# Kernel optimization log

Hardware: AMD Instinct MI355X
Metric: run time of the kernel (lower is better)

The kernel has to match this reference:

```python
import jax, jax.numpy as jnp
import numpy as np

B, T, D, H = 2, 4096, 768, 12
HD = D // H  # head_dim = 64


def setup_inputs() -> dict:
    key = jax.random.key(0)
    ks = jax.random.split(key, 6)
    s = 0.02
    return {
        "x": jax.random.normal(ks[0], (B, T, D), dtype=jnp.float32),
        "Wq": jax.random.normal(ks[1], (D, D), dtype=jnp.float32) * s,
        "Wk": jax.random.normal(ks[2], (D, D), dtype=jnp.float32) * s,
        "Wv": jax.random.normal(ks[3], (D, D), dtype=jnp.float32) * s,
        "Wo": jax.random.normal(ks[4], (D, D), dtype=jnp.float32) * s,
        "bo": jnp.zeros((D,), dtype=jnp.float32),
    }


def reference(x, Wq, Wk, Wv, Wo, bo):
    b, t, d = x.shape
    # QKV projections (no bias), reshape to [B, H, T, HD]
    def heads(w):
        return (x @ w.T).reshape(b, t, H, HD).transpose(0, 2, 1, 3)
    q, k, v = heads(Wq), heads(Wk), heads(Wv)
    scores = jnp.einsum("bhqd,bhkd->bhqk", q, k)  # [B,H,T,T]
    causal = jnp.tril(jnp.ones((t, t), dtype=bool))
    scores = jnp.where(causal, scores, -jnp.inf)
    attn = jax.nn.softmax(scores / jnp.sqrt(jnp.float32(HD)), axis=-1)
    ctx = jnp.einsum("bhqk,bhkd->bhqd", attn, v)  # [B,H,T,HD]
    ctx = ctx.transpose(0, 2, 1, 3).reshape(b, t, d)
    return ctx @ Wo.T + bo
```

## Files before the change

### kernel.cpp

```cpp
#include <hip/hip_runtime.h>
#include <hip/hip_bf16.h>
#include <cstdint>
#include <cstddef>

#define B_  2
#define T_  4096
#define D_  768
#define H_  12
#define HD_ 64
#define M_  (B_*T_)

#define SCL 0.18033688f

typedef __bf16 bf16x8 __attribute__((ext_vector_type(8)));
typedef float  f32x4  __attribute__((ext_vector_type(4)));
using bf16 = __hip_bfloat16;

__device__ inline float fexp2(float x) {
  float r; asm("v_exp_f32 %0, %1" : "=v"(r) : "v"(x)); return r;
}
__device__ inline uint32_t pkbf(float a, float b) {
  union { bf16 h[2]; uint32_t u; } x;
  x.h[0] = __float2bfloat16(a); x.h[1] = __float2bfloat16(b);
  return x.u;
}
#define GLD16(g, l) __builtin_amdgcn_global_load_lds( \
    (const __attribute__((address_space(1))) uint32_t*)(const void*)(g), \
    (__attribute__((address_space(3))) uint32_t*)(void*)(l), 16, 0, 0)

__global__ void cvt_x_kernel(const float* __restrict__ src, bf16* __restrict__ dst, int n4) {
  int i = blockIdx.x * blockDim.x + threadIdx.x;
  if (i < n4) {
    float4 v = ((const float4*)src)[i];
    union { bf16 o[4]; uint2 u; } pk;
    pk.o[0] = __float2bfloat16(v.x); pk.o[1] = __float2bfloat16(v.y);
    pk.o[2] = __float2bfloat16(v.z); pk.o[3] = __float2bfloat16(v.w);
    *(uint2*)(dst + 4 * (size_t)i) = pk.u;
  }
}

__global__ void cvt_w_kernel(const float* __restrict__ s0, const float* __restrict__ s1,
                             const float* __restrict__ s2, const float* __restrict__ s3,
                             bf16* __restrict__ d0, bf16* __restrict__ d1,
                             bf16* __restrict__ d2, bf16* __restrict__ d3, int n4) {
  const float* s; bf16* d;
  switch (blockIdx.y) {
    case 0: s = s0; d = d0; break;
    case 1: s = s1; d = d1; break;
    case 2: s = s2; d = d2; break;
    default: s = s3; d = d3; break;
  }
  int i = blockIdx.x * blockDim.x + threadIdx.x;
  if (i < n4) {
    float4 v = ((const float4*)s)[i];
    union { bf16 o[4]; uint2 u; } pk;
    pk.o[0] = __float2bfloat16(v.x); pk.o[1] = __float2bfloat16(v.y);
    pk.o[2] = __float2bfloat16(v.z); pk.o[3] = __float2bfloat16(v.w);
    *(uint2*)(d + 4 * (size_t)i) = pk.u;
  }
}

__global__ __launch_bounds__(256) void gemm_qkv(const bf16* __restrict__ A,
                                                const bf16* __restrict__ W0,
                                                const bf16* __restrict__ W1,
                                                const bf16* __restrict__ W2,
                                                bf16* __restrict__ O0,
                                                bf16* __restrict__ O1,
                                                bf16* __restrict__ O2t) {
  __shared__ bf16 As[128 * 40];
  __shared__ bf16 Bs[128 * 40];
  const int z = blockIdx.z;
  const bf16* Bw = (z == 0) ? W0 : ((z == 1) ? W1 : W2);
  const int t  = threadIdx.x;
  const int m0 = blockIdx.y * 128;
  const int n0 = blockIdx.x * 128;
  const int wid = t >> 6, lane = t & 63;
  const int wm = (wid >> 1) * 64, wn = (wid & 1) * 64;
  const int mi = lane & 15, qd = lane >> 4;

  f32x4 acc[4][4] = {};

  for (int k0 = 0; k0 < 768; k0 += 32) {
    __syncthreads();
    #pragma unroll
    for (int c = 0; c < 2; ++c) {
      int q   = t + 256 * c;
      int row = q >> 2, c16 = q & 3;
      uint4 va = *(const uint4*)(A  + (size_t)(m0 + row) * 768 + k0 + c16 * 8);
      *(uint4*)(As + row * 40 + c16 * 8) = va;
      uint4 vb = *(const uint4*)(Bw + (size_t)(n0 + row) * 768 + k0 + c16 * 8);
      *(uint4*)(Bs + row * 40 + c16 * 8) = vb;
    }
    __syncthreads();
    bf16x8 af[4], bfr[4];
    #pragma unroll
    for (int mt = 0; mt < 4; ++mt)
      af[mt] = *(const bf16x8*)(As + (wm + mt * 16 + mi) * 40 + qd * 8);
    #pragma unroll
    for (int nt = 0; nt < 4; ++nt)
      bfr[nt] = *(const bf16x8*)(Bs + (wn + nt * 16 + mi) * 40 + qd * 8);
    #pragma unroll
    for (int mt = 0; mt < 4; ++mt)
      #pragma unroll
      for (int nt = 0; nt < 4; ++nt)
        acc[mt][nt] = __builtin_amdgcn_mfma_f32_16x16x32_bf16(af[mt], bfr[nt], acc[mt][nt], 0, 0, 0);
  }

  const float scl = (z == 1) ? SCL : 1.0f;
  bf16* Ob = (z == 0) ? O0 : O1;
  #pragma unroll
  for (int mt = 0; mt < 4; ++mt) {
    #pragma unroll
    for (int nt = 0; nt < 4; ++nt) {
      int gr0 = m0 + wm + mt * 16 + qd * 4;
      int gc  = n0 + wn + nt * 16 + mi;
      if (z == 2) {
        union { bf16 o[4]; uint2 u; } pk;
        #pragma unroll
        for (int r = 0; r < 4; ++r) pk.o[r] = __float2bfloat16(acc[mt][nt][r]);
        int bb = gr0 >> 12, tt = gr0 & 4095;
        *(uint2*)(O2t + (size_t)bb * 768 * 4096 + (size_t)gc * 4096 + tt) = pk.u;
      } else {
        #pragma unroll
        for (int r = 0; r < 4; ++r)
          Ob[(size_t)(gr0 + r) * 768 + gc] = __float2bfloat16(acc[mt][nt][r] * scl);
      }
    }
  }
}

__global__ __launch_bounds__(256) void gemm_out(const bf16* __restrict__ A,
                                                const bf16* __restrict__ Bw,
                                                float* __restrict__ Cf,
                                                const float* __restrict__ bias) {
  __shared__ bf16 As[128 * 40];
  __shared__ bf16 Bs[128 * 40];
  const int t  = threadIdx.x;
  const int m0 = blockIdx.y * 128;
  const int n0 = blockIdx.x * 128;
  const int wid = t >> 6, lane = t & 63;
  const int wm = (wid >> 1) * 64, wn = (wid & 1) * 64;
  const int mi = lane & 15, qd = lane >> 4;

  f32x4 acc[4][4] = {};

  for (int k0 = 0; k0 < 768; k0 += 32) {
    __syncthreads();
    #pragma unroll
    for (int c = 0; c < 2; ++c) {
      int q   = t + 256 * c;
      int row = q >> 2, c16 = q & 3;
      uint4 va = *(const uint4*)(A  + (size_t)(m0 + row) * 768 + k0 + c16 * 8);
      *(uint4*)(As + row * 40 + c16 * 8) = va;
      uint4 vb = *(const uint4*)(Bw + (size_t)(n0 + row) * 768 + k0 + c16 * 8);
      *(uint4*)(Bs + row * 40 + c16 * 8) = vb;
    }
    __syncthreads();
    bf16x8 af[4], bfr[4];
    #pragma unroll
    for (int mt = 0; mt < 4; ++mt)
      af[mt] = *(const bf16x8*)(As + (wm + mt * 16 + mi) * 40 + qd * 8);
    #pragma unroll
    for (int nt = 0; nt < 4; ++nt)
      bfr[nt] = *(const bf16x8*)(Bs + (wn + nt * 16 + mi) * 40 + qd * 8);
    #pragma unroll
    for (int mt = 0; mt < 4; ++mt)
      #pragma unroll
      for (int nt = 0; nt < 4; ++nt)
        acc[mt][nt] = __builtin_amdgcn_mfma_f32_16x16x32_bf16(af[mt], bfr[nt], acc[mt][nt], 0, 0, 0);
  }

  #pragma unroll
  for (int mt = 0; mt < 4; ++mt)
    #pragma unroll
    for (int nt = 0; nt < 4; ++nt) {
      int gr0 = m0 + wm + mt * 16 + qd * 4;
      int gc  = n0 + wn + nt * 16 + mi;
      #pragma unroll
      for (int r = 0; r < 4; ++r)
        Cf[(size_t)(gr0 + r) * 768 + gc] = acc[mt][nt][r] + bias[gc];
    }
}

__global__ __launch_bounds__(256) void flash_attn(const bf16* __restrict__ Q,
                                                  const bf16* __restrict__ K,
                                                  const bf16* __restrict__ Vt,
                                                  bf16* __restrict__ ctx) {
  __shared__ bf16 Ks[2][4096];
  __shared__ bf16 Vs[2][4096];
  __shared__ bf16 Pt[4][32 * 72];
  const int t = threadIdx.x;
  const int w = t >> 6, lane = t & 63;
  const int mi = lane & 15, qd = lane >> 4;
  const int bh   = blockIdx.x % 24;
  const int qrev = blockIdx.x / 24;
  const int q0 = T_ - 128 - qrev * 128;
  const int b = bh / H_, h = bh % H_;
  const size_t bTD = (size_t)b * T_ * D_;
  const char* Kp = (const char*)(K  + bTD + (size_t)h * HD_);
  const char* Vp = (const char*)(Vt + (size_t)b * D_ * T_ + (size_t)h * HD_ * T_);
  const int qwmin = q0 + w * 32;

  int vkoff[2], vvoff[2];
  #pragma unroll
  for (int i = 0; i < 2; ++i) {
    int s  = i * 64 + lane;
    int rl = s >> 3, cs = s & 7;
    int c  = cs ^ (rl & 7);
    vkoff[i] = (w * 16 + rl) * 1536 + c * 16;
    vvoff[i] = (w * 16 + rl) * 8192 + c * 16;
  }

  int fidx[4][2];
  #pragma unroll
  for (int jt = 0; jt < 4; ++jt)
    #pragma unroll
    for (int kt = 0; kt < 2; ++kt)
      fidx[jt][kt] = (jt * 16 + mi) * 64 + (((kt * 4 + qd) ^ (mi & 7)) * 8);

  bf16x8 qf[2][2];
  const bf16* Qp = Q + bTD + (size_t)h * HD_;
  #pragma unroll
  for (int qt = 0; qt < 2; ++qt)
    #pragma unroll
    for (int kt = 0; kt < 2; ++kt)
      qf[qt][kt] = *(const bf16x8*)(Qp + (size_t)(qwmin + qt * 16 + mi) * D_ + kt * 32 + qd * 8);

  f32x4 oacc[4][2] = {};
  float lst[2] = {0.f, 0.f};

  const int ntiles = q0 / 64 + 2;

  #pragma unroll
  for (int i = 0; i < 2; ++i) {
    GLD16(Kp + vkoff[i], &Ks[0][w * 1024 + i * 512]);
    GLD16(Vp + vvoff[i], &Vs[0][w * 1024 + i * 512]);
  }

  for (int tt = 0; tt < ntiles; ++tt) {
    __syncthreads();
    const int par = tt & 1;
    if (tt + 1 < ntiles) {
      const size_t j1 = (size_t)(tt + 1) * 64;
      const int np = par ^ 1;
      #pragma unroll
      for (int i = 0; i < 2; ++i) {
        GLD16(Kp + vkoff[i] + j1 * 1536, &Ks[np][w * 1024 + i * 512]);
        GLD16(Vp + vvoff[i] + j1 * 2,    &Vs[np][w * 1024 + i * 512]);
      }
    }
    const int j0 = tt * 64;
    if (j0 > qwmin + 31) continue;

    f32x4 sacc[4][2] = {};
    #pragma unroll
    for (int jt = 0; jt < 4; ++jt)
      #pragma unroll
      for (int kt = 0; kt < 2; ++kt) {
        bf16x8 kf = *(const bf16x8*)&Ks[par][fidx[jt][kt]];
        #pragma unroll
        for (int qt = 0; qt < 2; ++qt)
          sacc[jt][qt] = __builtin_amdgcn_mfma_f32_16x16x32_bf16(kf, qf[qt][kt], sacc[jt][qt], 0, 0, 0);
      }

    if (j0 + 63 > qwmin) {
      #pragma unroll
      for (int jt = 0; jt < 4; ++jt)
        #pragma unroll
        for (int qt = 0; qt < 2; ++qt) {
          int qg = qwmin + qt * 16 + mi;
          #pragma unroll
          for (int r = 0; r < 4; ++r) {
            int jg = j0 + jt * 16 + qd * 4 + r;
            if (jg > qg) sacc[jt][qt][r] = -1e30f;
          }
        }
    }

    #pragma unroll
    for (int jt = 0; jt < 4; ++jt)
      #pragma unroll
      for (int qt = 0; qt < 2; ++qt) {
        float p0 = fexp2(sacc[jt][qt][0]);
        float p1 = fexp2(sacc[jt][qt][1]);
        float p2 = fexp2(sacc[jt][qt][2]);
        float p3 = fexp2(sacc[jt][qt][3]);
        lst[qt] += (p0 + p1) + (p2 + p3);
        union { uint32_t u[2]; uint64_t d; } pw;
        pw.u[0] = pkbf(p0, p1);
        pw.u[1] = pkbf(p2, p3);
        *(uint64_t*)&Pt[w][(qt * 16 + mi) * 72 + jt * 16 + qd * 4] = pw.d;
      }

    bf16x8 vf[4][2];
    #pragma unroll
    for (int dt = 0; dt < 4; ++dt)
      #pragma unroll
      for (int kt = 0; kt < 2; ++kt)
        vf[dt][kt] = *(const bf16x8*)&Vs[par][fidx[dt][kt]];

    asm volatile("s_waitcnt lgkmcnt(0)" ::: "memory");

    #pragma unroll
    for (int ktp = 0; ktp < 2; ++ktp)
      #pragma unroll
      for (int qt = 0; qt < 2; ++qt) {
        bf16x8 pf = *(const bf16x8*)&Pt[w][(qt * 16 + mi) * 72 + ktp * 32 + qd * 8];
        #pragma unroll
        for (int dt = 0; dt < 4; ++dt)
          oacc[dt][qt] = __builtin_amdgcn_mfma_f32_16x16x32_bf16(vf[dt][ktp], pf, oacc[dt][qt], 0, 0, 0);
      }
  }

  #pragma unroll
  for (int qt = 0; qt < 2; ++qt) {
    float l = lst[qt];
    l += __shfl_xor(l, 16);
    l += __shfl_xor(l, 32);
    float inv = __builtin_amdgcn_rcpf(l);
    int qg = qwmin + qt * 16 + mi;
    bf16* cp = ctx + bTD + (size_t)qg * D_ + h * HD_ + qd * 4;
    #pragma unroll
    for (int dt = 0; dt < 4; ++dt) {
      union { bf16 o[4]; uint2 u; } pko;
      #pragma unroll
      for (int r = 0; r < 4; ++r) pko.o[r] = __float2bfloat16(oacc[dt][qt][r] * inv);
      *(uint2*)(cp + dt * 16) = pko.u;
    }
  }
}

extern "C" void kernel_launch(void* const* d_in, const int* in_sizes, int n_in,
                              void* d_out, int out_size, void* d_ws, size_t ws_size,
                              hipStream_t stream) {
  const float* x  = (const float*)d_in[0];
  const float* Wq = (const float*)d_in[1];
  const float* Wk = (const float*)d_in[2];
  const float* Wv = (const float*)d_in[3];
  const float* Wo = (const float*)d_in[4];
  const float* bo = (const float*)d_in[5];
  float* out = (float*)d_out;

  char* ws = (char*)d_ws;
  const size_t SZ  = (size_t)M_ * D_ * 2;
  const size_t WSZ = (size_t)D_ * D_ * 2;
  bf16* xb   = (bf16*)(ws);
  bf16* Qb   = (bf16*)(ws + 1 * SZ);
  bf16* Kb   = (bf16*)(ws + 2 * SZ);
  bf16* Vtg  = (bf16*)(ws + 3 * SZ);
  bf16* ctxb = (bf16*)(ws + 4 * SZ);
  bf16* Wqb  = (bf16*)(ws + 5 * SZ);
  bf16* Wkb  = (bf16*)(ws + 5 * SZ + 1 * WSZ);
  bf16* Wvb  = (bf16*)(ws + 5 * SZ + 2 * WSZ);
  bf16* Wob  = (bf16*)(ws + 5 * SZ + 3 * WSZ);

  const int nx4 = M_ * D_ / 4;
  cvt_x_kernel<<<(nx4 + 255) / 256, 256, 0, stream>>>(x, xb, nx4);
  const int nw4 = D_ * D_ / 4;
  dim3 gcw((nw4 + 255) / 256, 4);
  cvt_w_kernel<<<gcw, 256, 0, stream>>>(Wq, Wk, Wv, Wo, Wqb, Wkb, Wvb, Wob, nw4);

  dim3 gq(D_ / 128, M_ / 128, 3);
  gemm_qkv<<<gq, 256, 0, stream>>>(xb, Wqb, Wkb, Wvb, Qb, Kb, Vtg);

  flash_attn<<<(T_ / 128) * B_ * H_, 256, 0, stream>>>(Qb, Kb, Vtg, ctxb);

  dim3 gg(D_ / 128, M_ / 128);
  gemm_out<<<gg, 256, 0, stream>>>(ctxb, Wob, out, bo);
}
```

Measured before the change: 280.9 us.

## Double-buffer GEMM tiles via async global-to-LDS loads, merge conversion kernels

```diff
diff --git a/kernel.cpp b/kernel.cpp
--- a/kernel.cpp
+++ b/kernel.cpp
@@ -19,36 +19,27 @@
 __device__ inline float fexp2(float x) {
   float r; asm("v_exp_f32 %0, %1" : "=v"(r) : "v"(x)); return r;
 }
-__device__ inline uint32_t pkbf(float a, float b) {
-  union { bf16 h[2]; uint32_t u; } x;
-  x.h[0] = __float2bfloat16(a); x.h[1] = __float2bfloat16(b);
-  return x.u;
+__device__ inline uint32_t fu(float x) { union { float f; uint32_t u; } c; c.f = x; return c.u; }
+__device__ inline uint32_t pktr(float a, float b) {
+  return __builtin_amdgcn_perm(fu(b), fu(a), 0x07060302);
 }
 #define GLD16(g, l) __builtin_amdgcn_global_load_lds( \
     (const __attribute__((address_space(1))) uint32_t*)(const void*)(g), \
     (__attribute__((address_space(3))) uint32_t*)(void*)(l), 16, 0, 0)
 
-__global__ void cvt_x_kernel(const float* __restrict__ src, bf16* __restrict__ dst, int n4) {
-  int i = blockIdx.x * blockDim.x + threadIdx.x;
-  if (i < n4) {
-    float4 v = ((const float4*)src)[i];
-    union { bf16 o[4]; uint2 u; } pk;
-    pk.o[0] = __float2bfloat16(v.x); pk.o[1] = __float2bfloat16(v.y);
-    pk.o[2] = __float2bfloat16(v.z); pk.o[3] = __float2bfloat16(v.w);
-    *(uint2*)(dst + 4 * (size_t)i) = pk.u;
-  }
-}
-
-__global__ void cvt_w_kernel(const float* __restrict__ s0, const float* __restrict__ s1,
-                             const float* __restrict__ s2, const float* __restrict__ s3,
-                             bf16* __restrict__ d0, bf16* __restrict__ d1,
-                             bf16* __restrict__ d2, bf16* __restrict__ d3, int n4) {
-  const float* s; bf16* d;
+__global__ void cvt_all(const float* __restrict__ x,
+                        const float* __restrict__ w0, const float* __restrict__ w1,
+                        const float* __restrict__ w2, const float* __restrict__ w3,
+                        bf16* __restrict__ xd,
+                        bf16* __restrict__ d0, bf16* __restrict__ d1,
+                        bf16* __restrict__ d2, bf16* __restrict__ d3) {
+  const float* s; bf16* d; int n4;
   switch (blockIdx.y) {
-    case 0: s = s0; d = d0; break;
-    case 1: s = s1; d = d1; break;
-    case 2: s = s2; d = d2; break;
-    default: s = s3; d = d3; break;
+    case 0: s = x;  d = xd; n4 = M_ * D_ / 4; break;
+    case 1: s = w0; d = d0; n4 = D_ * D_ / 4; break;
+    case 2: s = w1; d = d1; n4 = D_ * D_ / 4; break;
+    case 3: s = w2; d = d2; n4 = D_ * D_ / 4; break;
+    default: s = w3; d = d3; n4 = D_ * D_ / 4; break;
   }
   int i = blockIdx.x * blockDim.x + threadIdx.x;
   if (i < n4) {
@@ -67,38 +58,54 @@
                                                 bf16* __restrict__ O0,
                                                 bf16* __restrict__ O1,
                                                 bf16* __restrict__ O2t) {
-  __shared__ bf16 As[128 * 40];
-  __shared__ bf16 Bs[128 * 40];
+  __shared__ bf16 As[2][4096];
+  __shared__ bf16 Bs[2][4096];
   const int z = blockIdx.z;
-  const bf16* Bw = (z == 0) ? W0 : ((z == 1) ? W1 : W2);
+  const char* Bw = (const char*)((z == 0) ? W0 : ((z == 1) ? W1 : W2));
+  const char* Ap = (const char*)A;
   const int t  = threadIdx.x;
   const int m0 = blockIdx.y * 128;
   const int n0 = blockIdx.x * 128;
-  const int wid = t >> 6, lane = t & 63;
-  const int wm = (wid >> 1) * 64, wn = (wid & 1) * 64;
+  const int w = t >> 6, lane = t & 63;
+  const int wm = (w >> 1) * 64, wn = (w & 1) * 64;
   const int mi = lane & 15, qd = lane >> 4;
 
+  int aoff[2], boff[2];
+  #pragma unroll
+  for (int i = 0; i < 2; ++i) {
+    int L = i * 256 + t;
+    int row = L >> 2, sl = L & 3, c = sl ^ (row & 3);
+    aoff[i] = (m0 + row) * 1536 + c * 16;
+    boff[i] = (n0 + row) * 1536 + c * 16;
+  }
+  const int fsw = (qd ^ (mi & 3)) * 8;
+
   f32x4 acc[4][4] = {};
 
-  for (int k0 = 0; k0 < 768; k0 += 32) {
+  #pragma unroll
+  for (int i = 0; i < 2; ++i) {
+    GLD16(Ap + aoff[i], &As[0][i * 2048 + w * 512]);
+    GLD16(Bw + boff[i], &Bs[0][i * 2048 + w * 512]);
+  }
+
+  for (int kk = 0; kk < 24; ++kk) {
     __syncthreads();
-    #pragma unroll
-    for (int c = 0; c < 2; ++c) {
-      int q   = t + 256 * c;
-      int row = q >> 2, c16 = q & 3;
-      uint4 va = *(const uint4*)(A  + (size_t)(m0 + row) * 768 + k0 + c16 * 8);
-      *(uint4*)(As + row * 40 + c16 * 8) = va;
-      uint4 vb = *(const uint4*)(Bw + (size_t)(n0 + row) * 768 + k0 + c16 * 8);
-      *(uint4*)(Bs + row * 40 + c16 * 8) = vb;
-    }
-    __syncthreads();
+    const int par = kk & 1;
+    if (kk + 1 < 24) {
+      const int np = par ^ 1, kb = (kk + 1) * 64;
+      #pragma unroll
+      for (int i = 0; i < 2; ++i) {
+        GLD16(Ap + aoff[i] + kb, &As[np][i * 2048 + w * 512]);
+        GLD16(Bw + boff[i] + kb, &Bs[np][i * 2048 + w * 512]);
+      }
+    }
     bf16x8 af[4], bfr[4];
     #pragma unroll
     for (int mt = 0; mt < 4; ++mt)
-      af[mt] = *(const bf16x8*)(As + (wm + mt * 16 + mi) * 40 + qd * 8);
+      af[mt] = *(const bf16x8*)&As[par][(wm + mt * 16 + mi) * 32 + fsw];
     #pragma unroll
     for (int nt = 0; nt < 4; ++nt)
-      bfr[nt] = *(const bf16x8*)(Bs + (wn + nt * 16 + mi) * 40 + qd * 8);
+      bfr[nt] = *(const bf16x8*)&Bs[par][(wn + nt * 16 + mi) * 32 + fsw];
     #pragma unroll
     for (int mt = 0; mt < 4; ++mt)
       #pragma unroll
@@ -130,39 +137,56 @@
 }
 
 __global__ __launch_bounds__(256) void gemm_out(const bf16* __restrict__ A,
-                                                const bf16* __restrict__ Bw,
+                                                const bf16* __restrict__ Bw0,
                                                 float* __restrict__ Cf,
                                                 const float* __restrict__ bias) {
-  __shared__ bf16 As[128 * 40];
-  __shared__ bf16 Bs[128 * 40];
+  __shared__ bf16 As[2][4096];
+  __shared__ bf16 Bs[2][4096];
+  const char* Ap = (const char*)A;
+  const char* Bw = (const char*)Bw0;
   const int t  = threadIdx.x;
   const int m0 = blockIdx.y * 128;
   const int n0 = blockIdx.x * 128;
-  const int wid = t >> 6, lane = t & 63;
-  const int wm = (wid >> 1) * 64, wn = (wid & 1) * 64;
+  const int w = t >> 6, lane = t & 63;
+  const int wm = (w >> 1) * 64, wn = (w & 1) * 64;
   const int mi = lane & 15, qd = lane >> 4;
 
+  int aoff[2], boff[2];
+  #pragma unroll
+  for (int i = 0; i < 2; ++i) {
+    int L = i * 256 + t;
+    int row = L >> 2, sl = L & 3, c = sl ^ (row & 3);
+    aoff[i] = (m0 + row) * 1536 + c * 16;
+    boff[i] = (n0 + row) * 1536 + c * 16;
+  }
+  const int fsw = (qd ^ (mi & 3)) * 8;
+
   f32x4 acc[4][4] = {};
 
-  for (int k0 = 0; k0 < 768; k0 += 32) {
+  #pragma unroll
+  for (int i = 0; i < 2; ++i) {
+    GLD16(Ap + aoff[i], &As[0][i * 2048 + w * 512]);
+    GLD16(Bw + boff[i], &Bs[0][i * 2048 + w * 512]);
+  }
+
+  for (int kk = 0; kk < 24; ++kk) {
     __syncthreads();
-    #pragma unroll
-    for (int c = 0; c < 2; ++c) {
-      int q   = t + 256 * c;
-      int row = q >> 2, c16 = q & 3;
-      uint4 va = *(const uint4*)(A  + (size_t)(m0 + row) * 768 + k0 + c16 * 8);
-      *(uint4*)(As + row * 40 + c16 * 8) = va;
-      uint4 vb = *(const uint4*)(Bw + (size_t)(n0 + row) * 768 + k0 + c16 * 8);
-      *(uint4*)(Bs + row * 40 + c16 * 8) = vb;
-    }
-    __syncthreads();
+    const int par = kk & 1;
+    if (kk + 1 < 24) {
+      const int np = par ^ 1, kb = (kk + 1) * 64;
+      #pragma unroll
+      for (int i = 0; i < 2; ++i) {
+        GLD16(Ap + aoff[i] + kb, &As[np][i * 2048 + w * 512]);
+        GLD16(Bw + boff[i] + kb, &Bs[np][i * 2048 + w * 512]);
+      }
+    }
     bf16x8 af[4], bfr[4];
     #pragma unroll
     for (int mt = 0; mt < 4; ++mt)
-      af[mt] = *(const bf16x8*)(As + (wm + mt * 16 + mi) * 40 + qd * 8);
+      af[mt] = *(const bf16x8*)&As[par][(wm + mt * 16 + mi) * 32 + fsw];
     #pragma unroll
     for (int nt = 0; nt < 4; ++nt)
-      bfr[nt] = *(const bf16x8*)(Bs + (wn + nt * 16 + mi) * 40 + qd * 8);
+      bfr[nt] = *(const bf16x8*)&Bs[par][(wn + nt * 16 + mi) * 32 + fsw];
     #pragma unroll
     for (int mt = 0; mt < 4; ++mt)
       #pragma unroll
@@ -287,8 +311,8 @@
         float p3 = fexp2(sacc[jt][qt][3]);
         lst[qt] += (p0 + p1) + (p2 + p3);
         union { uint32_t u[2]; uint64_t d; } pw;
-        pw.u[0] = pkbf(p0, p1);
-        pw.u[1] = pkbf(p2, p3);
+        pw.u[0] = pktr(p0, p1);
+        pw.u[1] = pktr(p2, p3);
         *(uint64_t*)&Pt[w][(qt * 16 + mi) * 72 + jt * 16 + qd * 4] = pw.d;
       }
 
@@ -354,11 +378,8 @@
   bf16* Wvb  = (bf16*)(ws + 5 * SZ + 2 * WSZ);
   bf16* Wob  = (bf16*)(ws + 5 * SZ + 3 * WSZ);
 
-  const int nx4 = M_ * D_ / 4;
-  cvt_x_kernel<<<(nx4 + 255) / 256, 256, 0, stream>>>(x, xb, nx4);
-  const int nw4 = D_ * D_ / 4;
-  dim3 gcw((nw4 + 255) / 256, 4);
-  cvt_w_kernel<<<gcw, 256, 0, stream>>>(Wq, Wk, Wv, Wo, Wqb, Wkb, Wvb, Wob, nw4);
+  dim3 gcv(M_ * D_ / 4 / 256, 5);
+  cvt_all<<<gcv, 256, 0, stream>>>(x, Wq, Wk, Wv, Wo, xb, Wqb, Wkb, Wvb, Wob);
 
   dim3 gq(D_ / 128, M_ / 128, 3);
   gemm_qkv<<<gq, 256, 0, stream>>>(xb, Wqb, Wkb, Wvb, Qb, Kb, Vtg);
```

Result: faster. 266.0 us (-5.3%).
